# Kernel tuning notes

Measured on AMD Instinct MI355X. Metric: run time of the kernel, lower is better.

## Reference

```python
import jax, jax.numpy as jnp
import numpy as np
from jax import lax

BN_EPS = 1e-5


def _conv_bn_relu(x, W, b, gamma, beta):
    # x: [B, Cin, N]; W: [Cout, Cin]; 1x1 conv == channel GEMM
    y = jnp.einsum('oc,bcn->bon', W, x) + b[None, :, None]
    mean = jnp.mean(y, axis=(0, 2), keepdims=True)
    var = jnp.mean((y - mean) ** 2, axis=(0, 2), keepdims=True)  # biased, torch BN train mode
    y = gamma[None, :, None] * (y - mean) / jnp.sqrt(var + BN_EPS) + beta[None, :, None]
    return jax.nn.relu(y)


def setup_inputs() -> dict:
    key = jax.random.key(0)
    ks = jax.random.split(key, 8)
    B, N1, N2, C1, C2 = 16, 4096, 1024, 128, 256
    Cin, H = C1 + C2, 256  # MLP dims [384, 256, 256]
    inp = {
        'centroids1': jax.random.normal(ks[0], (B, 3, N1), jnp.float32),
        'centroids2': jax.random.normal(ks[1], (B, 3, N2), jnp.float32),
        'features1': jax.random.normal(ks[2], (B, C1, N1), jnp.float32),
        'features2': jax.random.normal(ks[3], (B, C2, N2), jnp.float32),
        'W1': jax.random.normal(ks[4], (H, Cin), jnp.float32) / np.sqrt(Cin),
        'b1': jnp.zeros((H,), jnp.float32),
        'g1': jnp.ones((H,), jnp.float32),
        'be1': jnp.zeros((H,), jnp.float32),
        'W2': jax.random.normal(ks[5], (H, H), jnp.float32) / np.sqrt(H),
        'b2': jnp.zeros((H,), jnp.float32),
        'g2': jnp.ones((H,), jnp.float32),
        'be2': jnp.zeros((H,), jnp.float32),
    }
    return inp


def reference(centroids1, centroids2, features1, features2,
              W1, b1, g1, be1, W2, b2, g2, be2):
    c1 = centroids1.transpose(0, 2, 1)  # [B, N1, 3]
    c2 = centroids2.transpose(0, 2, 1)  # [B, N2, 3]
    f2 = features2.transpose(0, 2, 1)   # [B, N2, C2]

    # pairwise squared distances [B, N1, N2]
    d = (jnp.sum(c1 ** 2, -1)[:, :, None] + jnp.sum(c2 ** 2, -1)[:, None, :]
         - 2.0 * jnp.einsum('bnd,bmd->bnm', c1, c2))

    # 3 nearest neighbors (smallest distances)
    neg_top, idx = lax.top_k(-d, 3)            # idx: [B, N1, 3]
    dist3 = -neg_top
    recip = 1.0 / (dist3 + 1e-8)
    weight = recip / jnp.sum(recip, axis=2, keepdims=True)  # [B, N1, 3]

    gathered = jax.vmap(lambda f, i: f[i])(f2, idx)         # [B, N1, 3, C2]
    interp = jnp.sum(gathered * weight[..., None], axis=2)  # [B, N1, C2]

    feats = jnp.concatenate((features1.transpose(0, 2, 1), interp), axis=-1)  # [B, N1, C1+C2]
    x = feats.transpose(0, 2, 1)  # [B, C1+C2, N1]
    x = _conv_bn_relu(x, W1, b1, g1, be1)
    x = _conv_bn_relu(x, W2, b2, g2, be2)
    return x  # [B, 256, N1]
```

## Files before the change

kernel.cpp:

```cpp
#include <hip/hip_runtime.h>
#include <math.h>

#define N1 4096
#define N2 1024
#define C1 128
#define C2 256
#define CIN 384
#define H 256
#define BATCH 16
#define BN_EPS 1e-5f

typedef __attribute__((ext_vector_type(8))) short bf16x8;
typedef __attribute__((ext_vector_type(4))) float f32x4;

__device__ inline float bf2f(short s) {
    union { unsigned u; float f; } x;
    x.u = ((unsigned)(unsigned short)s) << 16;
    return x.f;
}
__device__ inline short f2bf(float f) {
    union { float f; unsigned u; } x; x.f = f;
    unsigned r = x.u + 0x7fffu + ((x.u >> 16) & 1u);
    return (short)(r >> 16);
}

typedef const __attribute__((address_space(1))) unsigned int guint;
typedef __attribute__((address_space(3))) unsigned int luint;
__device__ inline void gll16(const void* g, void* l) {
    __builtin_amdgcn_global_load_lds((guint*)g, (luint*)l, 16, 0, 0);
}

__global__ __launch_bounds__(512)
void prep_fused(const float* __restrict__ c1, const float* __restrict__ c2,
                const float* __restrict__ f2, const float* __restrict__ W1,
                const float* __restrict__ W2,
                float4* __restrict__ pk, short* __restrict__ f2t,
                short* __restrict__ W1s, short* __restrict__ W2s) {
    __shared__ __align__(16) char lds_raw[29184];
    const int blk = blockIdx.x;
    const int t = threadIdx.x;

    if (blk < 1024) {
        float4* sc = (float4*)lds_raw;
        float*  md = (float*)(lds_raw + 16384);
        int*    mi = (int*)(lds_raw + 16384 + 6400);
        const int b = blk >> 6, ng = blk & 63;
        const float* c2b = c2 + (size_t)b * 3 * N2;
        for (int j = t; j < N2; j += 512) {
            float xx = c2b[j], yy = c2b[N2 + j], zz = c2b[2 * N2 + j];
            sc[j] = make_float4(-2.f * xx, -2.f * yy, -2.f * zz, xx * xx + yy * yy + zz * zz);
        }
        __syncthreads();

        const int q = t & 63;
        const int oct = t >> 6;
        const int n = ng * 64 + q;
        const float* c1b = c1 + (size_t)b * 3 * N1;
        const float x = c1b[n], y = c1b[N1 + n], z = c1b[2 * N1 + n];

        float d0 = 3.4e38f, d1 = 3.4e38f, d2 = 3.4e38f;
        int i0 = 0, i1 = 0, i2 = 0;
        const int j0 = oct * 128;
        #pragma unroll 8
        for (int jj = 0; jj < 128; ++jj) {
            const int j = j0 + jj;
            float4 cc = sc[j];
            float d = fmaf(x, cc.x, fmaf(y, cc.y, fmaf(z, cc.z, cc.w)));
            bool c0v = d < d0, c1v = d < d1, c2v = d < d2;
            i2 = c1v ? i1 : (c2v ? j : i2);
            i1 = c0v ? i0 : (c1v ? j : i1);
            i0 = c0v ? j  : i0;
            d2 = __builtin_amdgcn_fmed3f(d1, d2, d);
            d1 = __builtin_amdgcn_fmed3f(d0, d1, d);
            d0 = fminf(d0, d);
        }
        const int mb = q * 25 + oct * 3;
        md[mb + 0] = d0; md[mb + 1] = d1; md[mb + 2] = d2;
        mi[mb + 0] = i0; mi[mb + 1] = i1; mi[mb + 2] = i2;
        __syncthreads();

        if (t < 64) {
            float e0 = 3.4e38f, e1 = 3.4e38f, e2 = 3.4e38f;
            int a0 = 0, a1 = 0, a2 = 0;
            #pragma unroll
            for (int r = 0; r < 24; ++r) {
                const int rr = t * 25 + r;
                float d = md[rr]; int j = mi[rr];
                bool c0 = d < e0, c1v = d < e1, c2v = d < e2;
                e2 = c1v ? e1 : (c2v ? d : e2);  a2 = c1v ? a1 : (c2v ? j : a2);
                e1 = c0 ? e0 : (c1v ? d : e1);   a1 = c0 ? a0 : (c1v ? j : a1);
                e0 = c0 ? d  : e0;               a0 = c0 ? j  : a0;
            }
            const float s1 = x * x + y * y + z * z;
            float r0 = 1.0f / (e0 + s1 + 1e-8f);
            float r1 = 1.0f / (e1 + s1 + 1e-8f);
            float r2 = 1.0f / (e2 + s1 + 1e-8f);
            float rs = r0 + r1 + r2;
            unsigned pack = (unsigned)a0 | ((unsigned)a1 << 10) | ((unsigned)a2 << 20);
            pk[(size_t)b * N1 + n] = make_float4(__uint_as_float(pack), r0 / rs, r1 / rs, r2 / rs);
        }
    } else if (blk < 3072) {
        typedef float (*st_t)[32][33];
        st_t st = (st_t)lds_raw;
        const int half = t >> 8, tt = t & 255;
        const int tid = (blk - 1024) * 2 + half;
        const int j0 = (tid & 31) * 32, c0 = ((tid >> 5) & 7) * 32, b = tid >> 8;
        {
            const int cc = tt >> 3, jj = (tt & 7) * 4;
            const float* src = f2 + ((size_t)b * C2 + c0 + cc) * N2 + j0 + jj;
            float4 v = *(const float4*)src;
            st[half][cc][jj + 0] = v.x; st[half][cc][jj + 1] = v.y;
            st[half][cc][jj + 2] = v.z; st[half][cc][jj + 3] = v.w;
        }
        __syncthreads();
        {
            const int j = tt >> 3, cb = (tt & 7) * 4;
            short4 v = { f2bf(st[half][cb + 0][j]), f2bf(st[half][cb + 1][j]),
                         f2bf(st[half][cb + 2][j]), f2bf(st[half][cb + 3][j]) };
            *(short4*)(f2t + ((size_t)b * N2 + j0 + j) * C2 + c0 + cb) = v;
        }
    } else {
        const bool w1 = (blk < 3096);
        const int K = w1 ? CIN : H;
        const int nkb = K >> 3;
        const int id = (blk - (w1 ? 3072 : 3096)) * 512 + t;
        if (id < 256 * nkb) {
            const float* W = w1 ? W1 : W2;
            short* Wsw = w1 ? W1s : W2s;
            const int m = id / nkb, kb = id % nkb;
            const float* src = W + (size_t)m * K + kb * 8;
            bf16x8 v;
            #pragma unroll
            for (int j = 0; j < 8; ++j) v[j] = f2bf(src[j]);
            *(bf16x8*)(Wsw + ((size_t)kb * 256 + m) * 8) = v;
        }
    }
}

__global__ __launch_bounds__(256)
void gemm1_kernel(const short* __restrict__ Wsw,
                  const float* __restrict__ f1,
                  const short* __restrict__ f2t, const float4* __restrict__ pk,
                  short* __restrict__ Ykc, float2* __restrict__ P) {
    __shared__ __align__(16) short B_lds[48][64][8];

    const int t = threadIdx.x;
    const int blk = blockIdx.x;
    const int b = blk >> 6, nt = blk & 63;
    const int n0 = nt * 64;

    const int lane = t & 63, wv = t >> 6;
    const int wm = wv;
    const int l16 = lane & 15, lq = lane >> 4;

    const float* f1b = f1 + (size_t)b * C1 * N1;
    const int kbt = t >> 4, nq = (t & 15) * 4;
    float4 fv[8];
    #pragma unroll
    for (int e = 0; e < 8; ++e)
        fv[e] = *(const float4*)(f1b + (size_t)(kbt * 8 + e) * N1 + n0 + nq);

    {
        const int col = t & 63;
        const int kq  = t >> 6;
        float4 pv = pk[(size_t)b * N1 + n0 + col];
        unsigned u = __float_as_uint(pv.x);
        const short* rr0 = f2t + ((size_t)b * N2 + (u & 1023u)) * C2;
        const short* rr1 = f2t + ((size_t)b * N2 + ((u >> 10) & 1023u)) * C2;
        const short* rr2 = f2t + ((size_t)b * N2 + ((u >> 20) & 1023u)) * C2;
        #pragma unroll
        for (int i = 0; i < 8; ++i) {
            const int kbl = i * 4 + kq;
            bf16x8 g0 = *(const bf16x8*)(rr0 + kbl * 8);
            bf16x8 g1 = *(const bf16x8*)(rr1 + kbl * 8);
            bf16x8 g2 = *(const bf16x8*)(rr2 + kbl * 8);
            bf16x8 o;
            #pragma unroll
            for (int e = 0; e < 8; ++e)
                o[e] = f2bf(fmaf(pv.w, bf2f(g2[e]), fmaf(pv.z, bf2f(g1[e]), pv.y * bf2f(g0[e]))));
            *(bf16x8*)&B_lds[16 + kbl][col][0] = o;
        }
    }
    #pragma unroll
    for (int j = 0; j < 4; ++j) {
        bf16x8 pw;
        pw[0] = f2bf(j == 0 ? fv[0].x : j == 1 ? fv[0].y : j == 2 ? fv[0].z : fv[0].w);
        pw[1] = f2bf(j == 0 ? fv[1].x : j == 1 ? fv[1].y : j == 2 ? fv[1].z : fv[1].w);
        pw[2] = f2bf(j == 0 ? fv[2].x : j == 1 ? fv[2].y : j == 2 ? fv[2].z : fv[2].w);
        pw[3] = f2bf(j == 0 ? fv[3].x : j == 1 ? fv[3].y : j == 2 ? fv[3].z : fv[3].w);
        pw[4] = f2bf(j == 0 ? fv[4].x : j == 1 ? fv[4].y : j == 2 ? fv[4].z : fv[4].w);
        pw[5] = f2bf(j == 0 ? fv[5].x : j == 1 ? fv[5].y : j == 2 ? fv[5].z : fv[5].w);
        pw[6] = f2bf(j == 0 ? fv[6].x : j == 1 ? fv[6].y : j == 2 ? fv[6].z : fv[6].w);
        pw[7] = f2bf(j == 0 ? fv[7].x : j == 1 ? fv[7].y : j == 2 ? fv[7].z : fv[7].w);
        *(bf16x8*)&B_lds[kbt][nq + j][0] = pw;
    }
    __syncthreads();

    f32x4 acc[4][4];
    #pragma unroll
    for (int i = 0; i < 4; ++i)
        #pragma unroll
        for (int j = 0; j < 4; ++j)
            acc[i][j] = (f32x4){0.f, 0.f, 0.f, 0.f};

    bf16x8 aA[4], aB[4];
    auto loadA = [&](int s, bf16x8* dst) {
        const short* ap = Wsw + ((size_t)(s * 4 + lq) * 256 + wm * 64 + l16) * 8;
        #pragma unroll
        for (int f = 0; f < 4; ++f) dst[f] = *(const bf16x8*)(ap + (size_t)f * 16 * 8);
    };
    loadA(0, aA);
    __builtin_amdgcn_s_setprio(1);
    #pragma unroll
    for (int s = 0; s < 12; ++s) {
        bf16x8* acur = (s & 1) ? aB : aA;
        bf16x8* anxt = (s & 1) ? aA : aB;
        if (s + 1 < 12) loadA(s + 1, anxt);
        bf16x8 bb4[4];
        #pragma unroll
        for (int f = 0; f < 4; ++f)
            bb4[f] = *(const bf16x8*)&B_lds[s * 4 + lq][f * 16 + l16][0];
        #pragma unroll
        for (int i = 0; i < 4; ++i)
            #pragma unroll
            for (int j = 0; j < 4; ++j)
                acc[i][j] = __builtin_amdgcn_mfma_f32_16x16x32_bf16(acur[i], bb4[j], acc[i][j], 0, 0, 0);
    }
    __builtin_amdgcn_s_setprio(0);

    short* Yb = Ykc + (size_t)b * 32 * N1 * 8;
    #pragma unroll
    for (int i = 0; i < 4; ++i) {
        const int kb = wm * 8 + i * 2 + (lq >> 1);
        const int kr0 = (lq & 1) * 4;
        #pragma unroll
        for (int j = 0; j < 4; ++j) {
            const int n = n0 + j * 16 + l16;
            short4 v = { f2bf(acc[i][j][0]), f2bf(acc[i][j][1]),
                         f2bf(acc[i][j][2]), f2bf(acc[i][j][3]) };
            *(short4*)(Yb + ((size_t)kb * N1 + n) * 8 + kr0) = v;
        }
    }

    #pragma unroll
    for (int i = 0; i < 4; ++i) {
        #pragma unroll
        for (int r = 0; r < 4; ++r) {
            float s = 0.f, qq = 0.f;
            #pragma unroll
            for (int j = 0; j < 4; ++j) {
                float xv = acc[i][j][r];
                s += xv; qq += xv * xv;
            }
            #pragma unroll
            for (int msk = 1; msk < 16; msk <<= 1) {
                s  += __shfl_xor(s, msk);
                qq += __shfl_xor(qq, msk);
            }
            if (l16 == 0) {
                const int c = wm * 64 + i * 16 + lq * 4 + r;
                P[(size_t)c * 1024 + blk] = make_float2(s, qq);
            }
        }
    }
}

__global__ __launch_bounds__(256)
void gemm2_kernel(const short* __restrict__ Wsw, const short* __restrict__ y1kc,
                  const float* __restrict__ scale, const float* __restrict__ shift,
                  short* __restrict__ Ykc, float2* __restrict__ P) {
    __shared__ __align__(16) short B_lds[32][32][8];
    __shared__ float sc_s[256], sh_s[256];

    const int t = threadIdx.x;
    const int blk = blockIdx.x;
    const int b = blk >> 7, nt = blk & 127;
    const int n0 = nt * 32;

    const int lane = t & 63, wv = t >> 6;
    const int wm = wv;
    const int l16 = lane & 15, lq = lane >> 4;

    sc_s[t] = scale[t]; sh_s[t] = shift[t];

    #pragma unroll
    for (int i = 0; i < 4; ++i) {
        const int u = wv * 4 + i;
        const short* g = y1kc + (((size_t)b * 32 + u * 2 + (lane >> 5)) * N1 + n0 + (lane & 31)) * 8;
        gll16(g, &B_lds[u * 2][0][0]);
    }
    __syncthreads();

    f32x4 acc[4][2];
    #pragma unroll
    for (int i = 0; i < 4; ++i) {
        acc[i][0] = (f32x4){0.f, 0.f, 0.f, 0.f};
        acc[i][1] = (f32x4){0.f, 0.f, 0.f, 0.f};
    }

    bf16x8 aA[4], aB[4];
    auto loadA = [&](int s, bf16x8* dst) {
        const short* ap = Wsw + ((size_t)(s * 4 + lq) * 256 + wm * 64 + l16) * 8;
        #pragma unroll
        for (int f = 0; f < 4; ++f) dst[f] = *(const bf16x8*)(ap + (size_t)f * 16 * 8);
    };
    loadA(0, aA);
    __builtin_amdgcn_s_setprio(1);
    #pragma unroll
    for (int s = 0; s < 8; ++s) {
        bf16x8* acur = (s & 1) ? aB : aA;
        bf16x8* anxt = (s & 1) ? aA : aB;
        if (s + 1 < 8) loadA(s + 1, anxt);
        const int k0 = s * 32 + lq * 8;
        bf16x8 bb4[2];
        #pragma unroll
        for (int f = 0; f < 2; ++f) {
            bf16x8 raw = *(const bf16x8*)&B_lds[s * 4 + lq][f * 16 + l16][0];
            #pragma unroll
            for (int e = 0; e < 8; ++e)
                bb4[f][e] = f2bf(fmaxf(fmaf(bf2f(raw[e]), sc_s[k0 + e], sh_s[k0 + e]), 0.f));
        }
        #pragma unroll
        for (int i = 0; i < 4; ++i) {
            acc[i][0] = __builtin_amdgcn_mfma_f32_16x16x32_bf16(acur[i], bb4[0], acc[i][0], 0, 0, 0);
            acc[i][1] = __builtin_amdgcn_mfma_f32_16x16x32_bf16(acur[i], bb4[1], acc[i][1], 0, 0, 0);
        }
    }
    __builtin_amdgcn_s_setprio(0);

    short* Yb = Ykc + (size_t)b * 32 * N1 * 8;
    #pragma unroll
    for (int i = 0; i < 4; ++i) {
        const int kb = wm * 8 + i * 2 + (lq >> 1);
        const int kr0 = (lq & 1) * 4;
        #pragma unroll
        for (int j = 0; j < 2; ++j) {
            const int n = n0 + j * 16 + l16;
            short4 v = { f2bf(acc[i][j][0]), f2bf(acc[i][j][1]),
                         f2bf(acc[i][j][2]), f2bf(acc[i][j][3]) };
            *(short4*)(Yb + ((size_t)kb * N1 + n) * 8 + kr0) = v;
        }
    }

    #pragma unroll
    for (int i = 0; i < 4; ++i) {
        #pragma unroll
        for (int r = 0; r < 4; ++r) {
            float s = acc[i][0][r] + acc[i][1][r];
            float qq = acc[i][0][r] * acc[i][0][r] + acc[i][1][r] * acc[i][1][r];
            #pragma unroll
            for (int msk = 1; msk < 16; msk <<= 1) {
                s  += __shfl_xor(s, msk);
                qq += __shfl_xor(qq, msk);
            }
            if (l16 == 0) {
                const int c = wm * 64 + i * 16 + lq * 4 + r;
                P[(size_t)c * 2048 + blk] = make_float2(s, qq);
            }
        }
    }
}

template<int NP>
__global__ __launch_bounds__(256)
void bn_reduce(const float2* __restrict__ P, const float* __restrict__ g,
               const float* __restrict__ be, float* __restrict__ scale,
               float* __restrict__ shift) {
    const int c = blockIdx.x, t = threadIdx.x;
    float s = 0.f, q = 0.f;
    #pragma unroll
    for (int r = 0; r < NP / 256; ++r) {
        float2 v = P[(size_t)c * NP + r * 256 + t];
        s += v.x; q += v.y;
    }
    __shared__ float ss[256], sq[256];
    ss[t] = s; sq[t] = q;
    __syncthreads();
    for (int o = 128; o > 0; o >>= 1) {
        if (t < o) { ss[t] += ss[t + o]; sq[t] += sq[t + o]; }
        __syncthreads();
    }
    if (t == 0) {
        const float inv = 1.0f / (float)(BATCH * N1);
        float mean = ss[0] * inv;
        float var  = sq[0] * inv - mean * mean;
        float sc = g[c] / sqrtf(var + BN_EPS);
        scale[c] = sc;
        shift[c] = be[c] - mean * sc;
    }
}

__global__ __launch_bounds__(256)
void final_bn_relu(const short* __restrict__ y2kc, const float* __restrict__ scale,
                   const float* __restrict__ shift, float* __restrict__ out) {
    const int t = threadIdx.x;
    const int n0 = blockIdx.x * 1024 + t * 4;
    const int kb = blockIdx.y, b = blockIdx.z;
    const short* src = y2kc + ((size_t)(b * 32 + kb) * N1 + n0) * 8;
    bf16x8 v0 = *(const bf16x8*)(src);
    bf16x8 v1 = *(const bf16x8*)(src + 8);
    bf16x8 v2 = *(const bf16x8*)(src + 16);
    bf16x8 v3 = *(const bf16x8*)(src + 24);
    #pragma unroll
    for (int e = 0; e < 8; ++e) {
        const float sc = scale[kb * 8 + e], sh = shift[kb * 8 + e];
        float4 o;
        o.x = fmaxf(fmaf(bf2f(v0[e]), sc, sh), 0.f);
        o.y = fmaxf(fmaf(bf2f(v1[e]), sc, sh), 0.f);
        o.z = fmaxf(fmaf(bf2f(v2[e]), sc, sh), 0.f);
        o.w = fmaxf(fmaf(bf2f(v3[e]), sc, sh), 0.f);
        *(float4*)(out + ((size_t)(b * 256 + kb * 8 + e) * N1) + n0) = o;
    }
}

extern "C" void kernel_launch(void* const* d_in, const int* in_sizes, int n_in,
                              void* d_out, int out_size, void* d_ws, size_t ws_size,
                              hipStream_t stream) {
    const float* c1  = (const float*)d_in[0];
    const float* c2  = (const float*)d_in[1];
    const float* f1  = (const float*)d_in[2];
    const float* f2  = (const float*)d_in[3];
    const float* W1  = (const float*)d_in[4];
    const float* g1  = (const float*)d_in[6];
    const float* be1 = (const float*)d_in[7];
    const float* W2  = (const float*)d_in[8];
    const float* g2  = (const float*)d_in[10];
    const float* be2 = (const float*)d_in[11];
    float* out = (float*)d_out;

    char* ws = (char*)d_ws;
    short*  y1kc = (short*)ws;
    short*  f2t  = (short*)(ws + (32u << 20));
    short*  y2kc = (short*)(ws + (32u << 20));
    short*  W1s  = (short*)(ws + (64u << 20));
    short*  W2s  = (short*)(ws + (64u << 20) + (192u << 10));
    float4* pk   = (float4*)(ws + (64u << 20) + (512u << 10));
    float2* P1   = (float2*)(ws + (64u << 20) + (1536u << 10));
    float2* P2   = (float2*)(ws + (64u << 20) + (512u << 10));
    float* scale1 = (float*)(ws + (64u << 20) + (4608u << 10));
    float* shift1 = scale1 + 256;
    float* scale2 = shift1 + 256;
    float* shift2 = scale2 + 256;

    prep_fused<<<3112, 512, 0, stream>>>(c1, c2, f2, W1, W2, pk, f2t, W1s, W2s);

    gemm1_kernel<<<1024, 256, 0, stream>>>(W1s, f1, f2t, pk, y1kc, P1);
    bn_reduce<1024><<<256, 256, 0, stream>>>(P1, g1, be1, scale1, shift1);

    gemm2_kernel<<<2048, 256, 0, stream>>>(W2s, y1kc, scale1, shift1, y2kc, P2);
    bn_reduce<2048><<<256, 256, 0, stream>>>(P2, g2, be2, scale2, shift2);

    final_bn_relu<<<dim3(N1 / 1024, 32, BATCH), 256, 0, stream>>>(y2kc, scale2, shift2, out);
}
```

Baseline: 128.5 us.

## Warp-specialize gemm1 into producer/consumer waves with double-buffered LDS tiles

Turns gemm1 into a persistent kernel of 256 blocks with 512 threads. Four producer waves gather, interpolate and stage the B tile for the next tile into a second LDS buffer while four MFMA waves compute the current tile, so each block now processes four tiles. The goal is to hide the gather and global-load latency behind the MFMA work. The trade-offs are fewer blocks in flight, LDS use doubled to 96KB per block, and one __syncthreads per tile that serializes the two roles.

```diff
diff --git a/kernel.cpp b/kernel.cpp
--- a/kernel.cpp
+++ b/kernel.cpp
@@ -137,32 +137,32 @@
     }
 }
 
-__global__ __launch_bounds__(256)
+__global__ __launch_bounds__(512)
 void gemm1_kernel(const short* __restrict__ Wsw,
                   const float* __restrict__ f1,
                   const short* __restrict__ f2t, const float4* __restrict__ pk,
                   short* __restrict__ Ykc, float2* __restrict__ P) {
-    __shared__ __align__(16) short B_lds[48][64][8];
+    __shared__ __align__(16) short B_lds[2][48][64][8];
 
     const int t = threadIdx.x;
     const int blk = blockIdx.x;
-    const int b = blk >> 6, nt = blk & 63;
-    const int n0 = nt * 64;
-
-    const int lane = t & 63, wv = t >> 6;
-    const int wm = wv;
+    const int wid = t >> 6;
+    const bool is_compute = (wid < 4);
+    const int lane = t & 63;
     const int l16 = lane & 15, lq = lane >> 4;
-
-    const float* f1b = f1 + (size_t)b * C1 * N1;
-    const int kbt = t >> 4, nq = (t & 15) * 4;
-    float4 fv[8];
-    #pragma unroll
-    for (int e = 0; e < 8; ++e)
-        fv[e] = *(const float4*)(f1b + (size_t)(kbt * 8 + e) * N1 + n0 + nq);
-
-    {
-        const int col = t & 63;
-        const int kq  = t >> 6;
+    const int wm = wid & 3;
+    const int st = t & 255;
+
+    auto stage = [&](int tile, int bufi) {
+        const int b = tile >> 6, nt = tile & 63;
+        const int n0 = nt * 64;
+        const float* f1b = f1 + (size_t)b * C1 * N1;
+        const int kbt = st >> 4, nq = (st & 15) * 4;
+        float4 fv[8];
+        #pragma unroll
+        for (int e = 0; e < 8; ++e)
+            fv[e] = *(const float4*)(f1b + (size_t)(kbt * 8 + e) * N1 + n0 + nq);
+        const int col = st & 63, kq = st >> 6;
         float4 pv = pk[(size_t)b * N1 + n0 + col];
         unsigned u = __float_as_uint(pv.x);
         const short* rr0 = f2t + ((size_t)b * N2 + (u & 1023u)) * C2;
@@ -178,90 +178,104 @@
             #pragma unroll
             for (int e = 0; e < 8; ++e)
                 o[e] = f2bf(fmaf(pv.w, bf2f(g2[e]), fmaf(pv.z, bf2f(g1[e]), pv.y * bf2f(g0[e]))));
-            *(bf16x8*)&B_lds[16 + kbl][col][0] = o;
-        }
-    }
-    #pragma unroll
-    for (int j = 0; j < 4; ++j) {
-        bf16x8 pw;
-        pw[0] = f2bf(j == 0 ? fv[0].x : j == 1 ? fv[0].y : j == 2 ? fv[0].z : fv[0].w);
-        pw[1] = f2bf(j == 0 ? fv[1].x : j == 1 ? fv[1].y : j == 2 ? fv[1].z : fv[1].w);
-        pw[2] = f2bf(j == 0 ? fv[2].x : j == 1 ? fv[2].y : j == 2 ? fv[2].z : fv[2].w);
-        pw[3] = f2bf(j == 0 ? fv[3].x : j == 1 ? fv[3].y : j == 2 ? fv[3].z : fv[3].w);
-        pw[4] = f2bf(j == 0 ? fv[4].x : j == 1 ? fv[4].y : j == 2 ? fv[4].z : fv[4].w);
-        pw[5] = f2bf(j == 0 ? fv[5].x : j == 1 ? fv[5].y : j == 2 ? fv[5].z : fv[5].w);
-        pw[6] = f2bf(j == 0 ? fv[6].x : j == 1 ? fv[6].y : j == 2 ? fv[6].z : fv[6].w);
-        pw[7] = f2bf(j == 0 ? fv[7].x : j == 1 ? fv[7].y : j == 2 ? fv[7].z : fv[7].w);
-        *(bf16x8*)&B_lds[kbt][nq + j][0] = pw;
-    }
+            *(bf16x8*)&B_lds[bufi][16 + kbl][col][0] = o;
+        }
+        #pragma unroll
+        for (int j = 0; j < 4; ++j) {
+            bf16x8 pw;
+            pw[0] = f2bf(j == 0 ? fv[0].x : j == 1 ? fv[0].y : j == 2 ? fv[0].z : fv[0].w);
+            pw[1] = f2bf(j == 0 ? fv[1].x : j == 1 ? fv[1].y : j == 2 ? fv[1].z : fv[1].w);
+            pw[2] = f2bf(j == 0 ? fv[2].x : j == 1 ? fv[2].y : j == 2 ? fv[2].z : fv[2].w);
+            pw[3] = f2bf(j == 0 ? fv[3].x : j == 1 ? fv[3].y : j == 2 ? fv[3].z : fv[3].w);
+            pw[4] = f2bf(j == 0 ? fv[4].x : j == 1 ? fv[4].y : j == 2 ? fv[4].z : fv[4].w);
+            pw[5] = f2bf(j == 0 ? fv[5].x : j == 1 ? fv[5].y : j == 2 ? fv[5].z : fv[5].w);
+            pw[6] = f2bf(j == 0 ? fv[6].x : j == 1 ? fv[6].y : j == 2 ? fv[6].z : fv[6].w);
+            pw[7] = f2bf(j == 0 ? fv[7].x : j == 1 ? fv[7].y : j == 2 ? fv[7].z : fv[7].w);
+            *(bf16x8*)&B_lds[bufi][kbt][nq + j][0] = pw;
+        }
+    };
+
+    if (!is_compute) stage(blk, 0);
     __syncthreads();
 
-    f32x4 acc[4][4];
-    #pragma unroll
-    for (int i = 0; i < 4; ++i)
-        #pragma unroll
-        for (int j = 0; j < 4; ++j)
-            acc[i][j] = (f32x4){0.f, 0.f, 0.f, 0.f};
-
-    bf16x8 aA[4], aB[4];
-    auto loadA = [&](int s, bf16x8* dst) {
-        const short* ap = Wsw + ((size_t)(s * 4 + lq) * 256 + wm * 64 + l16) * 8;
-        #pragma unroll
-        for (int f = 0; f < 4; ++f) dst[f] = *(const bf16x8*)(ap + (size_t)f * 16 * 8);
-    };
-    loadA(0, aA);
-    __builtin_amdgcn_s_setprio(1);
-    #pragma unroll
-    for (int s = 0; s < 12; ++s) {
-        bf16x8* acur = (s & 1) ? aB : aA;
-        bf16x8* anxt = (s & 1) ? aA : aB;
-        if (s + 1 < 12) loadA(s + 1, anxt);
-        bf16x8 bb4[4];
-        #pragma unroll
-        for (int f = 0; f < 4; ++f)
-            bb4[f] = *(const bf16x8*)&B_lds[s * 4 + lq][f * 16 + l16][0];
-        #pragma unroll
-        for (int i = 0; i < 4; ++i)
-            #pragma unroll
-            for (int j = 0; j < 4; ++j)
-                acc[i][j] = __builtin_amdgcn_mfma_f32_16x16x32_bf16(acur[i], bb4[j], acc[i][j], 0, 0, 0);
-    }
-    __builtin_amdgcn_s_setprio(0);
-
-    short* Yb = Ykc + (size_t)b * 32 * N1 * 8;
-    #pragma unroll
-    for (int i = 0; i < 4; ++i) {
-        const int kb = wm * 8 + i * 2 + (lq >> 1);
-        const int kr0 = (lq & 1) * 4;
-        #pragma unroll
-        for (int j = 0; j < 4; ++j) {
-            const int n = n0 + j * 16 + l16;
-            short4 v = { f2bf(acc[i][j][0]), f2bf(acc[i][j][1]),
-                         f2bf(acc[i][j][2]), f2bf(acc[i][j][3]) };
-            *(short4*)(Yb + ((size_t)kb * N1 + n) * 8 + kr0) = v;
-        }
-    }
-
-    #pragma unroll
-    for (int i = 0; i < 4; ++i) {
-        #pragma unroll
-        for (int r = 0; r < 4; ++r) {
-            float s = 0.f, qq = 0.f;
-            #pragma unroll
-            for (int j = 0; j < 4; ++j) {
-                float xv = acc[i][j][r];
-                s += xv; qq += xv * xv;
-            }
-            #pragma unroll
-            for (int msk = 1; msk < 16; msk <<= 1) {
-                s  += __shfl_xor(s, msk);
-                qq += __shfl_xor(qq, msk);
-            }
-            if (l16 == 0) {
-                const int c = wm * 64 + i * 16 + lq * 4 + r;
-                P[(size_t)c * 1024 + blk] = make_float2(s, qq);
-            }
-        }
+    int buf = 0;
+    for (int ti = 0; ti < 4; ++ti) {
+        const int tile = blk + ti * 256;
+        if (is_compute) {
+            const int b = tile >> 6, nt = tile & 63;
+            const int n0 = nt * 64;
+
+            f32x4 acc[4][4];
+            #pragma unroll
+            for (int i = 0; i < 4; ++i)
+                #pragma unroll
+                for (int j = 0; j < 4; ++j)
+                    acc[i][j] = (f32x4){0.f, 0.f, 0.f, 0.f};
+
+            bf16x8 aA[4], aB[4];
+            auto loadA = [&](int s, bf16x8* dst) {
+                const short* ap = Wsw + ((size_t)(s * 4 + lq) * 256 + wm * 64 + l16) * 8;
+                #pragma unroll
+                for (int f = 0; f < 4; ++f) dst[f] = *(const bf16x8*)(ap + (size_t)f * 16 * 8);
+            };
+            loadA(0, aA);
+            __builtin_amdgcn_s_setprio(1);
+            #pragma unroll
+            for (int s = 0; s < 12; ++s) {
+                bf16x8* acur = (s & 1) ? aB : aA;
+                bf16x8* anxt = (s & 1) ? aA : aB;
+                if (s + 1 < 12) loadA(s + 1, anxt);
+                bf16x8 bb4[4];
+                #pragma unroll
+                for (int f = 0; f < 4; ++f)
+                    bb4[f] = *(const bf16x8*)&B_lds[buf][s * 4 + lq][f * 16 + l16][0];
+                #pragma unroll
+                for (int i = 0; i < 4; ++i)
+                    #pragma unroll
+                    for (int j = 0; j < 4; ++j)
+                        acc[i][j] = __builtin_amdgcn_mfma_f32_16x16x32_bf16(acur[i], bb4[j], acc[i][j], 0, 0, 0);
+            }
+            __builtin_amdgcn_s_setprio(0);
+
+            short* Yb = Ykc + (size_t)b * 32 * N1 * 8;
+            #pragma unroll
+            for (int i = 0; i < 4; ++i) {
+                const int kb = wm * 8 + i * 2 + (lq >> 1);
+                const int kr0 = (lq & 1) * 4;
+                #pragma unroll
+                for (int j = 0; j < 4; ++j) {
+                    const int n = n0 + j * 16 + l16;
+                    short4 v = { f2bf(acc[i][j][0]), f2bf(acc[i][j][1]),
+                                 f2bf(acc[i][j][2]), f2bf(acc[i][j][3]) };
+                    *(short4*)(Yb + ((size_t)kb * N1 + n) * 8 + kr0) = v;
+                }
+            }
+            #pragma unroll
+            for (int i = 0; i < 4; ++i) {
+                #pragma unroll
+                for (int r = 0; r < 4; ++r) {
+                    float s = 0.f, qq = 0.f;
+                    #pragma unroll
+                    for (int j = 0; j < 4; ++j) {
+                        float xv = acc[i][j][r];
+                        s += xv; qq += xv * xv;
+                    }
+                    #pragma unroll
+                    for (int msk = 1; msk < 16; msk <<= 1) {
+                        s  += __shfl_xor(s, msk);
+                        qq += __shfl_xor(qq, msk);
+                    }
+                    if (l16 == 0) {
+                        const int c = wm * 64 + i * 16 + lq * 4 + r;
+                        P[(size_t)c * 1024 + tile] = make_float2(s, qq);
+                    }
+                }
+            }
+        } else if (ti + 1 < 4) {
+            stage(blk + (ti + 1) * 256, buf ^ 1);
+        }
+        __syncthreads();
+        buf ^= 1;
     }
 }
 
@@ -444,7 +458,7 @@
 
     prep_fused<<<3112, 512, 0, stream>>>(c1, c2, f2, W1, W2, pk, f2t, W1s, W2s);
 
-    gemm1_kernel<<<1024, 256, 0, stream>>>(W1s, f1, f2t, pk, y1kc, P1);
+    gemm1_kernel<<<256, 512, 0, stream>>>(W1s, f1, f2t, pk, y1kc, P1);
     bn_reduce<1024><<<256, 256, 0, stream>>>(P1, g1, be1, scale1, shift1);
 
     gemm2_kernel<<<2048, 256, 0, stream>>>(W2s, y1kc, scale1, shift1, y2kc, P2);
```

Result: slower. 141.2 us (+9.9%).
